# Optimization experiments

Measured on AMD Instinct MI355X. Metric: run time of the kernel, lower is better.

The kernel has to match this reference:

```python
import jax, jax.numpy as jnp
import numpy as np

V, D, T, H = 32000, 1024, 1024, 16
HD = D // H  # head_size = 64
B = 4


def setup_inputs() -> dict:
    key = jax.random.key(0)
    ks = jax.random.split(key, 12)
    s = 0.02
    return {
        "idx": jax.random.randint(ks[0], (B, T), 0, V),
        "tok_emb": jax.random.normal(ks[1], (V, D), jnp.float32) * s,
        "pos_emb": jax.random.normal(ks[2], (T, D), jnp.float32) * s,
        "Wq": jax.random.normal(ks[3], (H, D, HD), jnp.float32) * s,
        "Wk": jax.random.normal(ks[4], (H, D, HD), jnp.float32) * s,
        "Wv": jax.random.normal(ks[5], (H, D, HD), jnp.float32) * s,
        "W1": jax.random.normal(ks[6], (D, D), jnp.float32) * s,
        "b1": jnp.zeros((D,), jnp.float32),
        "W2": jax.random.normal(ks[7], (D, D), jnp.float32) * s,
        "b2": jnp.zeros((D,), jnp.float32),
        "Wout": jax.random.normal(ks[8], (D, V), jnp.float32) * s,
        "bout": jnp.zeros((V,), jnp.float32),
    }


def reference(idx, tok_emb, pos_emb, Wq, Wk, Wv, W1, b1, W2, b2, Wout, bout):
    t = idx.shape[1]
    x = tok_emb[idx] + pos_emb[:t]  # [B,T,D]
    # per-head q,k,v projections (no bias), vectorized over heads
    q = jnp.einsum("btd,hde->bhte", x, Wq)
    k = jnp.einsum("btd,hde->bhte", x, Wk)
    v = jnp.einsum("btd,hde->bhte", x, Wv)
    scores = jnp.einsum("bhte,bhse->bhts", q, k) / jnp.sqrt(jnp.float32(HD))
    causal = jnp.tril(jnp.ones((t, t), bool))
    scores = jnp.where(causal, scores, -jnp.inf)
    w = jax.nn.softmax(scores, axis=-1)
    att = jnp.einsum("bhts,bhse->bhte", w, v)  # [B,H,T,HD]
    # concat heads along feature dim -> [B,T,D]
    out = att.transpose(0, 2, 1, 3).reshape(idx.shape[0], t, D)
    h = jax.nn.relu(out @ W1 + b1)
    h = jax.nn.relu(h @ W2 + b2)
    logits = h @ Wout + bout  # [B,T,V]
    return logits
```

## Files before the change

kernel.cpp:

```cpp
#include <hip/hip_runtime.h>
#include <cstdint>
#include <cstddef>


#define DEV __device__ __forceinline__

typedef __attribute__((ext_vector_type(8))) short bf16x8;
typedef __attribute__((ext_vector_type(4))) float f32x4;

DEV unsigned short f2bf(float f) {
  unsigned u = __float_as_uint(f);
  u = (u + 0x7fffu + ((u >> 16) & 1u)) >> 16;
  return (unsigned short)u;
}

DEV void stage16(const void* g, void* l) {
  __builtin_amdgcn_global_load_lds(
      (const __attribute__((address_space(1))) unsigned int*)g,
      (__attribute__((address_space(3))) unsigned int*)l, 16, 0, 0);
}

__global__ __launch_bounds__(256) void k_embed(
    const int* __restrict__ idx, const float* __restrict__ tok,
    const float* __restrict__ pos, unsigned short* __restrict__ xb) {
  int i = blockIdx.x * 256 + threadIdx.x;
  int row = i >> 8;
  int c4 = i & 255;
  int t = row & 1023;
  int tokid = idx[row];
  const float4 a = ((const float4*)tok)[(size_t)tokid * 256 + c4];
  const float4 p = ((const float4*)pos)[(size_t)t * 256 + c4];
  ushort4 o;
  o.x = f2bf(a.x + p.x); o.y = f2bf(a.y + p.y);
  o.z = f2bf(a.z + p.z); o.w = f2bf(a.w + p.w);
  ((ushort4*)xb)[i] = o;
}

__global__ __launch_bounds__(256) void k_pack_qkv(
    const float* __restrict__ Wq, const float* __restrict__ Wk,
    const float* __restrict__ Wv, unsigned short* __restrict__ out) {
  __shared__ float tile[64][65];
  int blk = blockIdx.x;
  int p = blk >> 8, h = (blk >> 4) & 15, d0 = (blk & 15) * 64;
  const float* W = (p == 0) ? Wq : ((p == 1) ? Wk : Wv);
  int tid = threadIdx.x, rq = tid >> 6, cc = tid & 63;
#pragma unroll
  for (int it = 0; it < 16; ++it) {
    int dr = it * 4 + rq;
    tile[dr][cc] = W[((size_t)h * 1024 + d0 + dr) * 64 + cc];
  }
  __syncthreads();
#pragma unroll
  for (int it = 0; it < 16; ++it) {
    int e = it * 4 + rq;
    out[((size_t)(p * 1024 + h * 64 + e)) * 1024 + d0 + cc] = f2bf(tile[cc][e]);
  }
}

__global__ __launch_bounds__(256) void k_transpose_all(
    const float* __restrict__ W1, const float* __restrict__ W2,
    const float* __restrict__ Wout, unsigned short* __restrict__ w1T,
    unsigned short* __restrict__ w2T, unsigned short* __restrict__ woutT) {
  __shared__ float tile[64][65];
  int b = blockIdx.x;
  const float* in;
  unsigned short* outp;
  int C, bx, by;
  if (b < 256)      { in = W1;   outp = w1T;   C = 1024;  bx = b & 15; by = b >> 4; }
  else if (b < 512) { b -= 256; in = W2;  outp = w2T;  C = 1024;  bx = b & 15; by = b >> 4; }
  else              { b -= 512; in = Wout; outp = woutT; C = 32000; bx = b % 500; by = b / 500; }
  const int R = 1024;
  const int c0 = bx * 64, r0 = by * 64;
  int tid = threadIdx.x, rq = tid >> 6, cc = tid & 63;
#pragma unroll
  for (int it = 0; it < 16; ++it) {
    int r = it * 4 + rq;
    tile[r][cc] = in[(size_t)(r0 + r) * C + c0 + cc];
  }
  __syncthreads();
#pragma unroll
  for (int it = 0; it < 16; ++it) {
    int c = it * 4 + rq;
    outp[(size_t)(c0 + c) * R + r0 + cc] = f2bf(tile[cc][c]);
  }
}

template <int EP>
__global__ __launch_bounds__(256, 2) void k_gemm128p(
    const unsigned short* __restrict__ A, const unsigned short* __restrict__ Bt,
    const float* __restrict__ bias, void* __restrict__ out0,
    void* __restrict__ out1, void* __restrict__ out2, int M, int N, int K) {
  __shared__ __align__(16) unsigned short sm[4 * 8192];
  const int tid = threadIdx.x;
  const int lane = tid & 63, w = tid >> 6;
  const int wr = w >> 1, wc = w & 1;
  const int fr = lane & 15, fg = lane >> 4;
  const int pch = (fg ^ ((fr >> 1) & 3)) << 3;

  const int nwg = gridDim.x * gridDim.y;
  int wg = blockIdx.y * gridDim.x + blockIdx.x;
  if ((nwg & 7) == 0) wg = (wg & 7) * (nwg >> 3) + (wg >> 3);
  const int m0 = (wg % gridDim.y) * 128;
  const int n0 = (wg / gridDim.y) * 128;

  const int srow = tid >> 2;
  const int sch = (((tid & 3) ^ ((srow >> 1) & 3))) * 8;
  const unsigned short* Ab0 = A + (size_t)(m0 + srow) * K + sch;
  const unsigned short* Ab1 = A + (size_t)(m0 + 64 + srow) * K + sch;
  const unsigned short* Bb0 = Bt + (size_t)(n0 + srow) * K + sch;
  const unsigned short* Bb1 = Bt + (size_t)(n0 + 64 + srow) * K + sch;
  const int NT = K >> 5;

#define STAGE_T(t, bb)                                                      \
  do {                                                                      \
    stage16(Ab0 + (t) * 32, &sm[(bb) * 8192 + tid * 8]);                    \
    stage16(Ab1 + (t) * 32, &sm[(bb) * 8192 + 2048 + tid * 8]);             \
    stage16(Bb0 + (t) * 32, &sm[(bb) * 8192 + 4096 + tid * 8]);             \
    stage16(Bb1 + (t) * 32, &sm[(bb) * 8192 + 6144 + tid * 8]);             \
  } while (0)

#define RD_ALL(dA, dB, bb)                                                  \
  do {                                                                      \
    const unsigned short* b_ = &sm[(bb) * 8192];                            \
    _Pragma("unroll") for (int m_ = 0; m_ < 4; ++m_)                        \
      dA[m_] = *(const bf16x8*)&b_[(wr * 64 + m_ * 16 + fr) * 32 + pch];    \
    _Pragma("unroll") for (int n_ = 0; n_ < 4; ++n_)                        \
      dB[n_] = *(const bf16x8*)&b_[4096 + (wc * 64 + n_ * 16 + fr) * 32 + pch]; \
  } while (0)

#define MFMA16(a, b)                                                        \
  do {                                                                      \
    __builtin_amdgcn_s_setprio(1);                                          \
    _Pragma("unroll") for (int m_ = 0; m_ < 4; ++m_)                        \
    _Pragma("unroll") for (int n_ = 0; n_ < 4; ++n_)                        \
      acc[m_][n_] = __builtin_amdgcn_mfma_f32_16x16x32_bf16(                \
          a[m_], b[n_], acc[m_][n_], 0, 0, 0);                              \
    __builtin_amdgcn_s_setprio(0);                                          \
  } while (0)

#define TB128(t, cA, cB, nA, nB)                                            \
  do {                                                                      \
    if ((t) + 3 < NT) STAGE_T((t) + 3, ((t) + 3) & 3);                      \
    if ((t) + 1 < NT) RD_ALL(nA, nB, ((t) + 1) & 3);                        \
    MFMA16(cA, cB);                                                         \
    if ((t) + 3 < NT) {                                                     \
      asm volatile("s_waitcnt vmcnt(4)" ::: "memory");                      \
    } else {                                                                \
      asm volatile("s_waitcnt vmcnt(0)" ::: "memory");                      \
    }                                                                       \
    __builtin_amdgcn_s_barrier();                                           \
  } while (0)

  f32x4 zero = {0.f, 0.f, 0.f, 0.f};
  f32x4 acc[4][4];
#pragma unroll
  for (int m = 0; m < 4; ++m)
#pragma unroll
    for (int n = 0; n < 4; ++n) acc[m][n] = zero;

  STAGE_T(0, 0); STAGE_T(1, 1); STAGE_T(2, 2);
  asm volatile("s_waitcnt vmcnt(4)" ::: "memory");
  __builtin_amdgcn_s_barrier();

  bf16x8 xA[4], xB[4], yA[4], yB[4];
  RD_ALL(xA, xB, 0);
  for (int t = 0; t < NT; t += 2) {
    TB128(t, xA, xB, yA, yB);
    TB128(t + 1, yA, yB, xA, xB);
  }
#undef STAGE_T
#undef RD_ALL
#undef MFMA16
#undef TB128

#pragma unroll
  for (int m = 0; m < 4; ++m) {
#pragma unroll
    for (int n = 0; n < 4; ++n) {
      const int rb = m0 + wr * 64 + m * 16 + fg * 4;
      const int cc = n0 + wc * 64 + n * 16 + fr;
#pragma unroll
      for (int i = 0; i < 4; ++i) {
        float v = acc[m][n][i];
        const int r = rb + i;
        if (EP == 1) {
          v += bias[cc];
          v = v > 0.f ? v : 0.f;
          ((unsigned short*)out0)[(size_t)r * N + cc] = f2bf(v);
        } else if (EP == 3) {
          int p = cc >> 10, rem = cc & 1023;
          int h = rem >> 6, e = rem & 63;
          int b = r >> 10, t2 = r & 1023;
          unsigned short* dst =
              (p == 0) ? (unsigned short*)out0
                       : ((p == 1) ? (unsigned short*)out1 : (unsigned short*)out2);
          dst[(((size_t)(b * 16 + h) * 1024) + t2) * 64 + e] = f2bf(v);
        }
      }
    }
  }
}

__global__ __launch_bounds__(512, 2) void k_gemm256(
    const unsigned short* __restrict__ A, const unsigned short* __restrict__ Bt,
    const float* __restrict__ bias, float* __restrict__ out,
    int M, int N, int K) {
  __shared__ __align__(16) unsigned short sm[4 * 16384];
  const int tid = threadIdx.x;
  const int lane = tid & 63, wid = tid >> 6;
  const int wr = wid >> 2, wc = wid & 3;
  const int fr = lane & 15, fg = lane >> 4;
  const int pch = (fg ^ ((fr >> 1) & 3)) << 3;

  const int nwg = gridDim.x * gridDim.y;
  int wg = blockIdx.y * gridDim.x + blockIdx.x;
  if ((nwg & 7) == 0) wg = (wg & 7) * (nwg >> 3) + (wg >> 3);
  const int m0 = (wg % gridDim.y) * 256;
  const int n0 = (wg / gridDim.y) * 256;

  const int srow = tid >> 2;
  const int scol = (((tid & 3) ^ ((srow >> 1) & 3))) * 8;
  const int NT = K >> 5;

#define STAGE_A(t, bb)                                                      \
  do {                                                                      \
    const unsigned short* g = A + (size_t)(m0 + srow) * K + (t) * 32 + scol; \
    stage16(g, &sm[(bb) * 16384 + tid * 8]);                                \
    stage16(g + (size_t)128 * K, &sm[(bb) * 16384 + 4096 + tid * 8]);       \
  } while (0)
#define STAGE_B(t, bb)                                                      \
  do {                                                                      \
    const unsigned short* g = Bt + (size_t)(n0 + srow) * K + (t) * 32 + scol; \
    stage16(g, &sm[(bb) * 16384 + 8192 + tid * 8]);                         \
    stage16(g + (size_t)128 * K, &sm[(bb) * 16384 + 8192 + 4096 + tid * 8]); \
  } while (0)

#define RD_G0(dA, dB, base)                                                 \
  do {                                                                      \
    _Pragma("unroll") for (int m_ = 0; m_ < 4; ++m_)                        \
      dA[m_] = *(const bf16x8*)&(base)[(wr * 128 + m_ * 16 + fr) * 32 + pch]; \
    _Pragma("unroll") for (int n_ = 0; n_ < 4; ++n_)                        \
      dB[n_] = *(const bf16x8*)&(base)[8192 + (wc * 64 + n_ * 16 + fr) * 32 + pch]; \
  } while (0)
#define RD_AHI(dA, base)                                                    \
  do {                                                                      \
    _Pragma("unroll") for (int m_ = 0; m_ < 4; ++m_)                        \
      dA[m_] = *(const bf16x8*)&(base)[(wr * 128 + (m_ + 4) * 16 + fr) * 32 + pch]; \
  } while (0)

#define MFMA_G(rbase, a, b)                                                 \
  do {                                                                      \
    __builtin_amdgcn_s_setprio(1);                                          \
    _Pragma("unroll") for (int m_ = 0; m_ < 4; ++m_)                        \
    _Pragma("unroll") for (int n_ = 0; n_ < 4; ++n_)                        \
      acc[(rbase) + m_][n_] = __builtin_amdgcn_mfma_f32_16x16x32_bf16(      \
          a[m_], b[n_], acc[(rbase) + m_][n_], 0, 0, 0);                    \
    __builtin_amdgcn_s_setprio(0);                                          \
  } while (0)

#define TILE_BODY(t, curA, curB, nxtA, nxtB)                                \
  do {                                                                      \
    const unsigned short* Ab_ = &sm[((t) & 3) * 16384];                     \
    bf16x8 a1_[4];                                                          \
    RD_AHI(a1_, Ab_);                                                       \
    if ((t) + 3 < NT) STAGE_A((t) + 3, ((t) + 3) & 3);                      \
    MFMA_G(0, curA, curB);                                                  \
    if ((t) + 1 < NT) {                                                     \
      const unsigned short* An_ = &sm[(((t) + 1) & 3) * 16384];             \
      RD_G0(nxtA, nxtB, An_);                                               \
    }                                                                       \
    if ((t) + 3 < NT) STAGE_B((t) + 3, ((t) + 3) & 3);                      \
    MFMA_G(4, a1_, curB);                                                   \
    if ((t) + 3 < NT) {                                                     \
      asm volatile("s_waitcnt vmcnt(4)" ::: "memory");                      \
    } else {                                                                \
      asm volatile("s_waitcnt vmcnt(0)" ::: "memory");                      \
    }                                                                       \
    __builtin_amdgcn_s_barrier();                                           \
  } while (0)

  f32x4 zero = {0.f, 0.f, 0.f, 0.f};
  f32x4 acc[8][4];
#pragma unroll
  for (int m = 0; m < 8; ++m)
#pragma unroll
    for (int n = 0; n < 4; ++n) acc[m][n] = zero;

  STAGE_A(0, 0); STAGE_B(0, 0);
  STAGE_A(1, 1); STAGE_B(1, 1);
  STAGE_A(2, 2); STAGE_B(2, 2);
  asm volatile("s_waitcnt vmcnt(4)" ::: "memory");
  __builtin_amdgcn_s_barrier();

  bf16x8 xA[4], xB[4], yA[4], yB[4];
  RD_G0(xA, xB, &sm[0]);

  for (int t = 0; t < NT; t += 2) {
    TILE_BODY(t, xA, xB, yA, yB);
    TILE_BODY(t + 1, yA, yB, xA, xB);
  }
#undef STAGE_A
#undef STAGE_B
#undef RD_G0
#undef RD_AHI
#undef MFMA_G
#undef TILE_BODY

  float* lds = (float*)sm;
  float bsv[4];
#pragma unroll
  for (int n = 0; n < 4; ++n) bsv[n] = bias[n0 + wc * 64 + n * 16 + fr];

  for (int m = 0; m < 8; ++m) {
#pragma unroll
    for (int n = 0; n < 4; ++n) {
      const int c = wc * 64 + n * 16 + fr;
#pragma unroll
      for (int i = 0; i < 4; ++i)
        lds[(wr * 16 + fg * 4 + i) * 260 + c] = acc[m][n][i] + bsv[n];
    }
    __syncthreads();
#pragma unroll
    for (int p = 0; p < 4; ++p) {
      const int rr = p * 8 + (tid >> 6);
      const int c4 = (tid & 63) * 4;
      f32x4 v = *(const f32x4*)&lds[rr * 260 + c4];
      const int grow = m0 + ((rr < 16) ? (m * 16 + rr) : (128 + m * 16 + rr - 16));
      __builtin_nontemporal_store(v, (f32x4*)&out[(size_t)grow * N + n0 + c4]);
    }
    __syncthreads();
  }
}

__global__ __launch_bounds__(256) void k_attn(
    const unsigned short* __restrict__ qb, const unsigned short* __restrict__ kb,
    const unsigned short* __restrict__ vb, unsigned short* __restrict__ attx) {
  __shared__ __align__(16) unsigned short Klds[64][72];
  __shared__ __align__(16) unsigned short Vt[64][72];
  __shared__ __align__(16) unsigned short Plds[2][4][16][72];
  const int wg = blockIdx.x;
  const int xcd = wg & 7, idxr = wg >> 3;
  const int bh = xcd * 8 + (idxr >> 3);
  const int qt = 7 - (idxr & 7);
  const int tid = threadIdx.x;
  const int w = tid >> 6, lane = tid & 63;
  const int fr = lane & 15, g = lane >> 4;
  const size_t base = (size_t)bh * (1024 * 64);
  const int qbase = qt * 128;

  bf16x8 qf[2][2];
#pragma unroll
  for (int qs = 0; qs < 2; ++qs)
#pragma unroll
    for (int t = 0; t < 2; ++t)
      qf[qs][t] = *(const bf16x8*)&qb[base +
          (size_t)(qbase + qs * 64 + w * 16 + fr) * 64 + t * 32 + g * 8];

  f32x4 zero = {0.f, 0.f, 0.f, 0.f};
  f32x4 o[2][4];
#pragma unroll
  for (int qs = 0; qs < 2; ++qs)
#pragma unroll
    for (int hb = 0; hb < 4; ++hb) o[qs][hb] = zero;
  float m_s[2] = {-3.0e38f, -3.0e38f}, l_s[2] = {0.f, 0.f};

  const int NTKV = 2 * qt + 2;
  for (int jt = 0; jt < NTKV; ++jt) {
    const int kvb = jt * 64;
#pragma unroll
    for (int it = 0; it < 2; ++it) {
      int c = tid + it * 256;
      int r = c >> 3, e0 = (c & 7) * 8;
      uint4 kd = *(const uint4*)&kb[base + (size_t)(kvb + r) * 64 + e0];
      *(uint4*)&Klds[r][e0] = kd;
      uint4 vd = *(const uint4*)&vb[base + (size_t)(kvb + r) * 64 + e0];
      const unsigned short* vs = (const unsigned short*)&vd;
#pragma unroll
      for (int j = 0; j < 8; ++j) Vt[e0 + j][r] = vs[j];
    }
    __syncthreads();

#pragma unroll
    for (int qs = 0; qs < 2; ++qs) {
      const int qlo = qbase + qs * 64;
      if (kvb > qlo + 63) continue;
      const int q_abs = qlo + w * 16 + fr;

      f32x4 st[4];
#pragma unroll
      for (int f = 0; f < 4; ++f) {
        st[f] = zero;
#pragma unroll
        for (int t = 0; t < 2; ++t) {
          bf16x8 kf = *(const bf16x8*)&Klds[f * 16 + fr][t * 32 + g * 8];
          st[f] = __builtin_amdgcn_mfma_f32_16x16x32_bf16(kf, qf[qs][t], st[f],
                                                          0, 0, 0);
        }
      }
      float sv[4][4];
      float tm = -3.0e38f;
#pragma unroll
      for (int f = 0; f < 4; ++f)
#pragma unroll
        for (int i = 0; i < 4; ++i) {
          int kv = kvb + f * 16 + g * 4 + i;
          float s = st[f][i] * 0.125f;
          if (kv > q_abs) s = -3.0e38f;
          sv[f][i] = s;
          tm = fmaxf(tm, s);
        }
      tm = fmaxf(tm, __shfl_xor(tm, 16));
      tm = fmaxf(tm, __shfl_xor(tm, 32));
      float mnew = fmaxf(m_s[qs], tm);
      float scale = expf(m_s[qs] - mnew);
      float lsum = 0.f;
#pragma unroll
      for (int f = 0; f < 4; ++f)
#pragma unroll
        for (int i = 0; i < 4; ++i) {
          float pv = expf(sv[f][i] - mnew);
          lsum += pv;
          Plds[qs][w][fr][f * 16 + g * 4 + i] = f2bf(pv);
        }
      lsum += __shfl_xor(lsum, 16);
      lsum += __shfl_xor(lsum, 32);
      l_s[qs] = l_s[qs] * scale + lsum;
      m_s[qs] = mnew;
#pragma unroll
      for (int i = 0; i < 4; ++i) {
        float sc = __shfl(scale, g * 4 + i);
#pragma unroll
        for (int hb = 0; hb < 4; ++hb) o[qs][hb][i] *= sc;
      }
      asm volatile("s_waitcnt lgkmcnt(0)" ::: "memory");
      __builtin_amdgcn_sched_barrier(0);
#pragma unroll
      for (int t = 0; t < 2; ++t) {
        bf16x8 pf = *(const bf16x8*)&Plds[qs][w][fr][t * 32 + g * 8];
#pragma unroll
        for (int hb = 0; hb < 4; ++hb) {
          bf16x8 vf = *(const bf16x8*)&Vt[hb * 16 + fr][t * 32 + g * 8];
          o[qs][hb] = __builtin_amdgcn_mfma_f32_16x16x32_bf16(pf, vf, o[qs][hb],
                                                              0, 0, 0);
        }
      }
    }
    __syncthreads();
  }

  const int b = bh >> 4, h = bh & 15;
#pragma unroll
  for (int qs = 0; qs < 2; ++qs) {
    const float inv = 1.f / l_s[qs];
#pragma unroll
    for (int i = 0; i < 4; ++i) {
      float sc = __shfl(inv, g * 4 + i);
      int trow = qbase + qs * 64 + w * 16 + g * 4 + i;
      size_t rowoff = ((size_t)(b * 1024 + trow)) * 1024 + h * 64;
#pragma unroll
      for (int hb = 0; hb < 4; ++hb)
        attx[rowoff + hb * 16 + fr] = f2bf(o[qs][hb][i] * sc);
    }
  }
}

extern "C" void kernel_launch(void* const* d_in, const int* in_sizes, int n_in,
                              void* d_out, int out_size, void* d_ws,
                              size_t ws_size, hipStream_t stream) {
  const int* idx = (const int*)d_in[0];
  const float* tok = (const float*)d_in[1];
  const float* pos = (const float*)d_in[2];
  const float* Wq = (const float*)d_in[3];
  const float* Wk = (const float*)d_in[4];
  const float* Wv = (const float*)d_in[5];
  const float* W1 = (const float*)d_in[6];
  const float* b1 = (const float*)d_in[7];
  const float* W2 = (const float*)d_in[8];
  const float* b2 = (const float*)d_in[9];
  const float* Wout = (const float*)d_in[10];
  const float* bout = (const float*)d_in[11];
  float* out = (float*)d_out;

  char* ws = (char*)d_ws;
  unsigned short* xb    = (unsigned short*)(ws + 0);
  unsigned short* wqkvT = (unsigned short*)(ws + 8388608);
  unsigned short* w1T   = (unsigned short*)(ws + 14680064);
  unsigned short* w2T   = (unsigned short*)(ws + 16777216);
  unsigned short* woutT = (unsigned short*)(ws + 18874368);
  unsigned short* qbuf  = (unsigned short*)(ws + 84410368);
  unsigned short* kbuf  = (unsigned short*)(ws + 92798976);
  unsigned short* vbuf  = (unsigned short*)(ws + 101187584);
  unsigned short* attx  = (unsigned short*)(ws + 109576192);
  unsigned short* h1    = (unsigned short*)(ws + 117964800);
  unsigned short* h2    = xb;

  k_embed<<<4096, 256, 0, stream>>>(idx, tok, pos, xb);
  k_pack_qkv<<<768, 256, 0, stream>>>(Wq, Wk, Wv, wqkvT);
  k_transpose_all<<<8512, 256, 0, stream>>>(W1, W2, Wout, w1T, w2T, woutT);

  k_gemm128p<3><<<dim3(24, 32), 256, 0, stream>>>(xb, wqkvT, nullptr, qbuf,
                                                  kbuf, vbuf, 4096, 3072, 1024);
  k_attn<<<512, 256, 0, stream>>>(qbuf, kbuf, vbuf, attx);
  k_gemm128p<1><<<dim3(8, 32), 256, 0, stream>>>(attx, w1T, b1, h1, nullptr,
                                                 nullptr, 4096, 1024, 1024);
  k_gemm128p<1><<<dim3(8, 32), 256, 0, stream>>>(h1, w2T, b2, h2, nullptr,
                                                 nullptr, 4096, 1024, 1024);
  k_gemm256<<<dim3(125, 16), 512, 0, stream>>>(h2, woutT, bout, out, 4096,
                                               32000, 1024);
}
```

Before: 461.3 us.

## Merge embed with QKV packing and overlap QKV GEMM with weight transposes

Combines the embedding and QKV weight packing into one launch, and puts the QKV projection GEMM and the W1/W2/Wout transpose-to-bf16 work into a single heterogeneous launch, with blocks branching on blockIdx. This removes two kernel launches and lets the memory-bound transpose blocks run alongside the compute-bound GEMM blocks. In exchange, the combined kernel allocates 64KB of LDS for every block, which may lower occupancy for the transpose blocks. The GEMM tile scheduling is also hardcoded for the QKV shape.

```diff
diff --git a/kernel.cpp b/kernel.cpp
--- a/kernel.cpp
+++ b/kernel.cpp
@@ -20,30 +20,32 @@
       (__attribute__((address_space(3))) unsigned int*)l, 16, 0, 0);
 }
 
-__global__ __launch_bounds__(256) void k_embed(
+__global__ __launch_bounds__(256) void k_prep(
     const int* __restrict__ idx, const float* __restrict__ tok,
-    const float* __restrict__ pos, unsigned short* __restrict__ xb) {
-  int i = blockIdx.x * 256 + threadIdx.x;
-  int row = i >> 8;
-  int c4 = i & 255;
-  int t = row & 1023;
-  int tokid = idx[row];
-  const float4 a = ((const float4*)tok)[(size_t)tokid * 256 + c4];
-  const float4 p = ((const float4*)pos)[(size_t)t * 256 + c4];
-  ushort4 o;
-  o.x = f2bf(a.x + p.x); o.y = f2bf(a.y + p.y);
-  o.z = f2bf(a.z + p.z); o.w = f2bf(a.w + p.w);
-  ((ushort4*)xb)[i] = o;
-}
-
-__global__ __launch_bounds__(256) void k_pack_qkv(
+    const float* __restrict__ pos, unsigned short* __restrict__ xb,
     const float* __restrict__ Wq, const float* __restrict__ Wk,
-    const float* __restrict__ Wv, unsigned short* __restrict__ out) {
+    const float* __restrict__ Wv, unsigned short* __restrict__ wqkvT) {
   __shared__ float tile[64][65];
-  int blk = blockIdx.x;
+  int b = blockIdx.x;
+  int tid = threadIdx.x;
+  if (b < 4096) {
+    int i = b * 256 + tid;
+    int row = i >> 8;
+    int c4 = i & 255;
+    int t = row & 1023;
+    int tokid = idx[row];
+    const float4 a = ((const float4*)tok)[(size_t)tokid * 256 + c4];
+    const float4 p = ((const float4*)pos)[(size_t)t * 256 + c4];
+    ushort4 o;
+    o.x = f2bf(a.x + p.x); o.y = f2bf(a.y + p.y);
+    o.z = f2bf(a.z + p.z); o.w = f2bf(a.w + p.w);
+    ((ushort4*)xb)[i] = o;
+    return;
+  }
+  int blk = b - 4096;
   int p = blk >> 8, h = (blk >> 4) & 15, d0 = (blk & 15) * 64;
   const float* W = (p == 0) ? Wq : ((p == 1) ? Wk : Wv);
-  int tid = threadIdx.x, rq = tid >> 6, cc = tid & 63;
+  int rq = tid >> 6, cc = tid & 63;
 #pragma unroll
   for (int it = 0; it < 16; ++it) {
     int dr = it * 4 + rq;
@@ -53,55 +55,59 @@
 #pragma unroll
   for (int it = 0; it < 16; ++it) {
     int e = it * 4 + rq;
-    out[((size_t)(p * 1024 + h * 64 + e)) * 1024 + d0 + cc] = f2bf(tile[cc][e]);
-  }
-}
-
-__global__ __launch_bounds__(256) void k_transpose_all(
+    wqkvT[((size_t)(p * 1024 + h * 64 + e)) * 1024 + d0 + cc] = f2bf(tile[cc][e]);
+  }
+}
+
+__global__ __launch_bounds__(256, 2) void k_qkv_tr(
+    const unsigned short* __restrict__ A, const unsigned short* __restrict__ Bt,
+    unsigned short* __restrict__ qbuf, unsigned short* __restrict__ kbuf,
+    unsigned short* __restrict__ vbuf,
     const float* __restrict__ W1, const float* __restrict__ W2,
     const float* __restrict__ Wout, unsigned short* __restrict__ w1T,
     unsigned short* __restrict__ w2T, unsigned short* __restrict__ woutT) {
-  __shared__ float tile[64][65];
+  __shared__ __align__(16) unsigned char sraw[65536];
+  const int tid = threadIdx.x;
   int b = blockIdx.x;
-  const float* in;
-  unsigned short* outp;
-  int C, bx, by;
-  if (b < 256)      { in = W1;   outp = w1T;   C = 1024;  bx = b & 15; by = b >> 4; }
-  else if (b < 512) { b -= 256; in = W2;  outp = w2T;  C = 1024;  bx = b & 15; by = b >> 4; }
-  else              { b -= 512; in = Wout; outp = woutT; C = 32000; bx = b % 500; by = b / 500; }
-  const int R = 1024;
-  const int c0 = bx * 64, r0 = by * 64;
-  int tid = threadIdx.x, rq = tid >> 6, cc = tid & 63;
-#pragma unroll
-  for (int it = 0; it < 16; ++it) {
-    int r = it * 4 + rq;
-    tile[r][cc] = in[(size_t)(r0 + r) * C + c0 + cc];
-  }
-  __syncthreads();
-#pragma unroll
-  for (int it = 0; it < 16; ++it) {
-    int c = it * 4 + rq;
-    outp[(size_t)(c0 + c) * R + r0 + cc] = f2bf(tile[cc][c]);
-  }
-}
-
-template <int EP>
-__global__ __launch_bounds__(256, 2) void k_gemm128p(
-    const unsigned short* __restrict__ A, const unsigned short* __restrict__ Bt,
-    const float* __restrict__ bias, void* __restrict__ out0,
-    void* __restrict__ out1, void* __restrict__ out2, int M, int N, int K) {
-  __shared__ __align__(16) unsigned short sm[4 * 8192];
-  const int tid = threadIdx.x;
+
+  if (b >= 768) {
+    b -= 768;
+    const float* in;
+    unsigned short* outp;
+    int C, bx, by;
+    if (b < 256)      { in = W1;   outp = w1T;   C = 1024;  bx = b & 15; by = b >> 4; }
+    else if (b < 512) { b -= 256; in = W2;  outp = w2T;  C = 1024;  bx = b & 15; by = b >> 4; }
+    else              { b -= 512; in = Wout; outp = woutT; C = 32000; bx = b % 500; by = b / 500; }
+    const int R = 1024;
+    const int c0 = bx * 64, r0 = by * 64;
+    float* tile = (float*)sraw;
+    int rq = tid >> 6, cc = tid & 63;
+#pragma unroll
+    for (int it = 0; it < 16; ++it) {
+      int r = it * 4 + rq;
+      tile[r * 65 + cc] = in[(size_t)(r0 + r) * C + c0 + cc];
+    }
+    __syncthreads();
+#pragma unroll
+    for (int it = 0; it < 16; ++it) {
+      int c = it * 4 + rq;
+      outp[(size_t)(c0 + c) * R + r0 + cc] = f2bf(tile[cc * 65 + c]);
+    }
+    return;
+  }
+
+  const int M = 4096, N = 3072, K = 1024;
+  unsigned short* sm = (unsigned short*)sraw;
   const int lane = tid & 63, w = tid >> 6;
   const int wr = w >> 1, wc = w & 1;
   const int fr = lane & 15, fg = lane >> 4;
   const int pch = (fg ^ ((fr >> 1) & 3)) << 3;
 
-  const int nwg = gridDim.x * gridDim.y;
-  int wg = blockIdx.y * gridDim.x + blockIdx.x;
-  if ((nwg & 7) == 0) wg = (wg & 7) * (nwg >> 3) + (wg >> 3);
-  const int m0 = (wg % gridDim.y) * 128;
-  const int n0 = (wg / gridDim.y) * 128;
+  const int nwg = 768;
+  int wg = b;
+  wg = (wg & 7) * (nwg >> 3) + (wg >> 3);
+  const int m0 = (wg % 32) * 128;
+  const int n0 = (wg / 32) * 128;
 
   const int srow = tid >> 2;
   const int sch = (((tid & 3) ^ ((srow >> 1) & 3))) * 8;
@@ -183,19 +189,114 @@
       for (int i = 0; i < 4; ++i) {
         float v = acc[m][n][i];
         const int r = rb + i;
-        if (EP == 1) {
-          v += bias[cc];
-          v = v > 0.f ? v : 0.f;
-          ((unsigned short*)out0)[(size_t)r * N + cc] = f2bf(v);
-        } else if (EP == 3) {
-          int p = cc >> 10, rem = cc & 1023;
-          int h = rem >> 6, e = rem & 63;
-          int b = r >> 10, t2 = r & 1023;
-          unsigned short* dst =
-              (p == 0) ? (unsigned short*)out0
-                       : ((p == 1) ? (unsigned short*)out1 : (unsigned short*)out2);
-          dst[(((size_t)(b * 16 + h) * 1024) + t2) * 64 + e] = f2bf(v);
-        }
+        int p = cc >> 10, rem = cc & 1023;
+        int h = rem >> 6, e = rem & 63;
+        int bb2 = r >> 10, t2 = r & 1023;
+        unsigned short* dst = (p == 0) ? qbuf : ((p == 1) ? kbuf : vbuf);
+        dst[(((size_t)(bb2 * 16 + h) * 1024) + t2) * 64 + e] = f2bf(v);
+      }
+    }
+  }
+}
+
+__global__ __launch_bounds__(256, 2) void k_gemm128p(
+    const unsigned short* __restrict__ A, const unsigned short* __restrict__ Bt,
+    const float* __restrict__ bias, unsigned short* __restrict__ out0,
+    int M, int N, int K) {
+  __shared__ __align__(16) unsigned short sm[4 * 8192];
+  const int tid = threadIdx.x;
+  const int lane = tid & 63, w = tid >> 6;
+  const int wr = w >> 1, wc = w & 1;
+  const int fr = lane & 15, fg = lane >> 4;
+  const int pch = (fg ^ ((fr >> 1) & 3)) << 3;
+
+  const int nwg = gridDim.x * gridDim.y;
+  int wg = blockIdx.y * gridDim.x + blockIdx.x;
+  if ((nwg & 7) == 0) wg = (wg & 7) * (nwg >> 3) + (wg >> 3);
+  const int m0 = (wg % gridDim.y) * 128;
+  const int n0 = (wg / gridDim.y) * 128;
+
+  const int srow = tid >> 2;
+  const int sch = (((tid & 3) ^ ((srow >> 1) & 3))) * 8;
+  const unsigned short* Ab0 = A + (size_t)(m0 + srow) * K + sch;
+  const unsigned short* Ab1 = A + (size_t)(m0 + 64 + srow) * K + sch;
+  const unsigned short* Bb0 = Bt + (size_t)(n0 + srow) * K + sch;
+  const unsigned short* Bb1 = Bt + (size_t)(n0 + 64 + srow) * K + sch;
+  const int NT = K >> 5;
+
+#define STAGE_T(t, bb)                                                      \
+  do {                                                                      \
+    stage16(Ab0 + (t) * 32, &sm[(bb) * 8192 + tid * 8]);                    \
+    stage16(Ab1 + (t) * 32, &sm[(bb) * 8192 + 2048 + tid * 8]);             \
+    stage16(Bb0 + (t) * 32, &sm[(bb) * 8192 + 4096 + tid * 8]);             \
+    stage16(Bb1 + (t) * 32, &sm[(bb) * 8192 + 6144 + tid * 8]);             \
+  } while (0)
+
+#define RD_ALL(dA, dB, bb)                                                  \
+  do {                                                                      \
+    const unsigned short* b_ = &sm[(bb) * 8192];                            \
+    _Pragma("unroll") for (int m_ = 0; m_ < 4; ++m_)                        \
+      dA[m_] = *(const bf16x8*)&b_[(wr * 64 + m_ * 16 + fr) * 32 + pch];    \
+    _Pragma("unroll") for (int n_ = 0; n_ < 4; ++n_)                        \
+      dB[n_] = *(const bf16x8*)&b_[4096 + (wc * 64 + n_ * 16 + fr) * 32 + pch]; \
+  } while (0)
+
+#define MFMA16(a, b)                                                        \
+  do {                                                                      \
+    __builtin_amdgcn_s_setprio(1);                                          \
+    _Pragma("unroll") for (int m_ = 0; m_ < 4; ++m_)                        \
+    _Pragma("unroll") for (int n_ = 0; n_ < 4; ++n_)                        \
+      acc[m_][n_] = __builtin_amdgcn_mfma_f32_16x16x32_bf16(                \
+          a[m_], b[n_], acc[m_][n_], 0, 0, 0);                              \
+    __builtin_amdgcn_s_setprio(0);                                          \
+  } while (0)
+
+#define TB128(t, cA, cB, nA, nB)                                            \
+  do {                                                                      \
+    if ((t) + 3 < NT) STAGE_T((t) + 3, ((t) + 3) & 3);                      \
+    if ((t) + 1 < NT) RD_ALL(nA, nB, ((t) + 1) & 3);                        \
+    MFMA16(cA, cB);                                                         \
+    if ((t) + 3 < NT) {                                                     \
+      asm volatile("s_waitcnt vmcnt(4)" ::: "memory");                      \
+    } else {                                                                \
+      asm volatile("s_waitcnt vmcnt(0)" ::: "memory");                      \
+    }                                                                       \
+    __builtin_amdgcn_s_barrier();                                           \
+  } while (0)
+
+  f32x4 zero = {0.f, 0.f, 0.f, 0.f};
+  f32x4 acc[4][4];
+#pragma unroll
+  for (int m = 0; m < 4; ++m)
+#pragma unroll
+    for (int n = 0; n < 4; ++n) acc[m][n] = zero;
+
+  STAGE_T(0, 0); STAGE_T(1, 1); STAGE_T(2, 2);
+  asm volatile("s_waitcnt vmcnt(4)" ::: "memory");
+  __builtin_amdgcn_s_barrier();
+
+  bf16x8 xA[4], xB[4], yA[4], yB[4];
+  RD_ALL(xA, xB, 0);
+  for (int t = 0; t < NT; t += 2) {
+    TB128(t, xA, xB, yA, yB);
+    TB128(t + 1, yA, yB, xA, xB);
+  }
+#undef STAGE_T
+#undef RD_ALL
+#undef MFMA16
+#undef TB128
+
+#pragma unroll
+  for (int m = 0; m < 4; ++m) {
+#pragma unroll
+    for (int n = 0; n < 4; ++n) {
+      const int rb = m0 + wr * 64 + m * 16 + fg * 4;
+      const int cc = n0 + wc * 64 + n * 16 + fr;
+#pragma unroll
+      for (int i = 0; i < 4; ++i) {
+        float v = acc[m][n][i] + bias[cc];
+        v = v > 0.f ? v : 0.f;
+        out0[(size_t)(rb + i) * N + cc] = f2bf(v);
       }
     }
   }
@@ -494,17 +595,14 @@
   unsigned short* h1    = (unsigned short*)(ws + 117964800);
   unsigned short* h2    = xb;
 
-  k_embed<<<4096, 256, 0, stream>>>(idx, tok, pos, xb);
-  k_pack_qkv<<<768, 256, 0, stream>>>(Wq, Wk, Wv, wqkvT);
-  k_transpose_all<<<8512, 256, 0, stream>>>(W1, W2, Wout, w1T, w2T, woutT);
-
-  k_gemm128p<3><<<dim3(24, 32), 256, 0, stream>>>(xb, wqkvT, nullptr, qbuf,
-                                                  kbuf, vbuf, 4096, 3072, 1024);
+  k_prep<<<4864, 256, 0, stream>>>(idx, tok, pos, xb, Wq, Wk, Wv, wqkvT);
+  k_qkv_tr<<<9280, 256, 0, stream>>>(xb, wqkvT, qbuf, kbuf, vbuf,
+                                     W1, W2, Wout, w1T, w2T, woutT);
   k_attn<<<512, 256, 0, stream>>>(qbuf, kbuf, vbuf, attx);
-  k_gemm128p<1><<<dim3(8, 32), 256, 0, stream>>>(attx, w1T, b1, h1, nullptr,
-                                                 nullptr, 4096, 1024, 1024);
-  k_gemm128p<1><<<dim3(8, 32), 256, 0, stream>>>(h1, w2T, b2, h2, nullptr,
-                                                 nullptr, 4096, 1024, 1024);
+  k_gemm128p<<<dim3(8, 32), 256, 0, stream>>>(attx, w1T, b1, h1, 4096, 1024,
+                                              1024);
+  k_gemm128p<<<dim3(8, 32), 256, 0, stream>>>(h1, w2T, b2, h2, 4096, 1024,
+                                              1024);
   k_gemm256<<<dim3(125, 16), 512, 0, stream>>>(h2, woutT, bout, out, 4096,
                                                32000, 1024);
 }
```

Result: no change. 470.5 us (+2.0%).
